# Kernel tuning notes

Measured on AMD Instinct MI355X. Metric: run time of the kernel, lower is better.

The kernel has to match this reference:

```python
import jax, jax.numpy as jnp
import numpy as np

EMBED_DIM = 128
NUM_HEADS = 4
HEAD_DIM = EMBED_DIM // NUM_HEADS


def setup_inputs() -> dict:
    key = jax.random.key(0)
    ks = jax.random.split(key, 12)
    B, N, D = 4, 4096, EMBED_DIM
    s = 1.0 / np.sqrt(D)
    inp = {
        "query": jax.random.normal(ks[0], (B, N, D), dtype=jnp.float32),
        "key": jax.random.normal(ks[1], (B, N, D), dtype=jnp.float32),
        "value": jax.random.normal(ks[2], (B, N, D), dtype=jnp.float32),
        "Wq": jax.random.uniform(ks[3], (D, D), jnp.float32, -s, s),
        "bq": jax.random.uniform(ks[4], (D,), jnp.float32, -s, s),
        "Wk": jax.random.uniform(ks[5], (D, D), jnp.float32, -s, s),
        "bk": jax.random.uniform(ks[6], (D,), jnp.float32, -s, s),
        "Wv": jax.random.uniform(ks[7], (D, D), jnp.float32, -s, s),
        "bv": jax.random.uniform(ks[8], (D,), jnp.float32, -s, s),
        "Wo": jax.random.uniform(ks[9], (D, D), jnp.float32, -s, s),
        "bo": jax.random.uniform(ks[10], (D,), jnp.float32, -s, s),
    }
    return inp


def reference(query, key, value, Wq, bq, Wk, bk, Wv, bv, Wo, bo):
    B, N, D = query.shape
    H, Dh = NUM_HEADS, HEAD_DIM
    scale = Dh ** -0.5
    # Linear projections (torch Linear: x @ W.T + b), split heads -> [B, H, N, Dh]
    Q = (query @ Wq.T + bq).reshape(B, N, H, Dh).transpose(0, 2, 1, 3)
    K = (key @ Wk.T + bk).reshape(B, N, H, Dh).transpose(0, 2, 1, 3)
    V = (value @ Wv.T + bv).reshape(B, N, H, Dh).transpose(0, 2, 1, 3)
    # Attention scores [B, H, N, N]
    scores = jnp.einsum('bhqd,bhkd->bhqk', Q, K) * scale
    attn = jax.nn.softmax(scores, axis=-1)
    ctx = jnp.einsum('bhqk,bhkd->bhqd', attn, V)  # [B, H, N, Dh]
    ctx = ctx.transpose(0, 2, 1, 3).reshape(B, N, D)
    return ctx @ Wo.T + bo
```

## Files before the change

kernel.cpp:

```cpp
#include <hip/hip_runtime.h>
#include <hip/hip_bf16.h>

#define N_SEQ 4096
#define DIM   128
#define NH    4
#define DH    32
#define BATCH 4

#define QSCALE 0.25503495870989204f

typedef __bf16 bf16x8 __attribute__((ext_vector_type(8)));
typedef __bf16 bf16x2 __attribute__((ext_vector_type(2)));
typedef __bf16 bf16x4 __attribute__((ext_vector_type(4)));
typedef float  f32x4  __attribute__((ext_vector_type(4)));

#define MFMA(a, b, c) __builtin_amdgcn_mfma_f32_16x16x32_bf16((a), (b), (c), 0, 0, 0)

static __device__ __forceinline__ bf16x8 cvt8(const float* __restrict__ p) {
    const float4* f4 = reinterpret_cast<const float4*>(p);
    float4 a = f4[0], b = f4[1];
    bf16x8 r;
    r[0] = (__bf16)a.x; r[1] = (__bf16)a.y; r[2] = (__bf16)a.z; r[3] = (__bf16)a.w;
    r[4] = (__bf16)b.x; r[5] = (__bf16)b.y; r[6] = (__bf16)b.z; r[7] = (__bf16)b.w;
    return r;
}

static __device__ __forceinline__ f32x4 exp4(f32x4 s) {
    f32x4 r;
    r[0] = __builtin_amdgcn_exp2f(s[0]);
    r[1] = __builtin_amdgcn_exp2f(s[1]);
    r[2] = __builtin_amdgcn_exp2f(s[2]);
    r[3] = __builtin_amdgcn_exp2f(s[3]);
    return r;
}

static __device__ __forceinline__ bf16x8 pack8(f32x4 a, f32x4 b) {
    bf16x8 o;
    o[0] = (__bf16)a[0]; o[1] = (__bf16)a[1];
    o[2] = (__bf16)a[2]; o[3] = (__bf16)a[3];
    o[4] = (__bf16)b[0]; o[5] = (__bf16)b[1];
    o[6] = (__bf16)b[2]; o[7] = (__bf16)b[3];
    return o;
}

__global__ __launch_bounds__(256) void cvt_w(
    const float* __restrict__ Wq, const float* __restrict__ Wk,
    const float* __restrict__ Wv, const float* __restrict__ Wo,
    __bf16* __restrict__ Wb)
{
    const int i = blockIdx.x * 256 + threadIdx.x;
    const int w = i >> 11;
    const int off = (i & 2047) * 8;
    const float* s = (w == 0) ? Wq : ((w == 1) ? Wk : ((w == 2) ? Wv : Wo));
    *(bf16x8*)(Wb + w * 16384 + off) = cvt8(s + off);
}

__global__ __launch_bounds__(256) void proj_qkv(
    const float* __restrict__ xq, const float* __restrict__ xk, const float* __restrict__ xv,
    const __bf16* __restrict__ Wb,
    const float* __restrict__ bq, const float* __restrict__ bk, const float* __restrict__ bv,
    __bf16* __restrict__ Qs, __bf16* __restrict__ Kb, __bf16* __restrict__ Vt)
{
    const int z = blockIdx.z;
    const float* x    = (z == 0) ? xq : ((z == 1) ? xk : xv);
    const __bf16* Wf  = Wb + z * 16384;
    const float* bias = (z == 0) ? bq : ((z == 1) ? bk : bv);
    const int b    = blockIdx.y;
    const int tid  = threadIdx.x;
    const int wave = tid >> 6, lane = tid & 63;
    const int quad = lane >> 4, l15 = lane & 15;
    const int n0   = blockIdx.x * 64 + wave * 16;

    bf16x8 a[4];
    const float* xrow = x + (b * N_SEQ + n0 + l15) * DIM + quad * 8;
    a[0] = cvt8(xrow);      a[1] = cvt8(xrow + 32);
    a[2] = cvt8(xrow + 64); a[3] = cvt8(xrow + 96);

    const int n = n0 + l15;
    #pragma unroll
    for (int t = 0; t < 8; t++) {
        const __bf16* wr = Wf + (t * 16 + l15) * DIM + quad * 8;
        bf16x8 w0 = *(const bf16x8*)(wr);
        bf16x8 w1 = *(const bf16x8*)(wr + 32);
        bf16x8 w2 = *(const bf16x8*)(wr + 64);
        bf16x8 w3 = *(const bf16x8*)(wr + 96);

        f32x4 acc = {0.f, 0.f, 0.f, 0.f};
        acc = MFMA(w0, a[0], acc);
        acc = MFMA(w1, a[1], acc);
        acc = MFMA(w2, a[2], acc);
        acc = MFMA(w3, a[3], acc);

        const int d0 = t * 16 + quad * 4;
        if (z == 0) {
            const int h = d0 >> 5, dh0 = d0 & 31;
            bf16x4 q4;
            #pragma unroll
            for (int r = 0; r < 4; r++)
                q4[r] = (__bf16)((acc[r] + bias[d0 + r]) * QSCALE);
            *(bf16x4*)(Qs + ((b * NH + h) * N_SEQ + n) * DH + dh0) = q4;
        } else if (z == 1) {
            const int h = d0 >> 5, dh0 = d0 & 31;
            bf16x4 k4;
            #pragma unroll
            for (int r = 0; r < 4; r++)
                k4[r] = (__bf16)(acc[r] + bias[d0 + r]);
            *(bf16x4*)(Kb + ((b * NH + h) * N_SEQ + n) * DH + dh0) = k4;
        } else {
            const int nl = n & 63;
            const int np = (n & ~63) | (nl & 35) | ((nl & 12) << 1) | ((nl & 16) >> 2);
            #pragma unroll
            for (int r = 0; r < 4; r++) {
                const int d = d0 + r, h = d >> 5, dh = d & 31;
                Vt[((b * NH + h) * DH + dh) * N_SEQ + np] = (__bf16)(acc[r] + bias[d]);
            }
        }
    }
}

__global__ __launch_bounds__(256, 2) void flash_attn(
    const __bf16* __restrict__ Qs, const __bf16* __restrict__ Kb,
    const __bf16* __restrict__ Vt, __bf16* __restrict__ ctxb)
{
    __shared__ __align__(16) char smem[77824];
    char* const Kbase = smem;
    char* const Vbase = smem + 40960;

    const int bid  = blockIdx.x;
    const int bh   = bid & 15;
    const int qc   = bid >> 4;
    const int tid  = threadIdx.x;
    const int wave = tid >> 6, lane = tid & 63;
    const int quad = lane >> 4, l15 = lane & 15;
    const int qh   = wave & 1, kh = wave >> 1;
    const int n0   = qc * 128 + qh * 64;
    const int KH   = 2048;

    const __bf16* Qp = Qs + (bh * N_SEQ + n0) * DH;
    bf16x8 qf[4];
    #pragma unroll
    for (int q = 0; q < 4; q++)
        qf[q] = *(const bf16x8*)(Qp + (q * 16 + l15) * DH + quad * 8);

    bf16x8 ones;
    #pragma unroll
    for (int i = 0; i < 8; i++) ones[i] = (__bf16)1.0f;

    const int r_ = tid >> 2, c_ = tid & 3;
    const __bf16* gK = Kb + (size_t)bh * N_SEQ * DH + r_ * DH + c_ * 8;
    const __bf16* gV = Vt + ((size_t)bh * DH + (tid >> 3)) * N_SEQ + (tid & 7) * 8;
    const int kofsK = r_ * 80 + c_ * 16;
    const int kofsV = (tid >> 3) * 144 + (tid & 7) * 16;

    {
        #pragma unroll
        for (int g = 0; g < 2; g++) {
            #pragma unroll
            for (int t = 0; t < 2; t++) {
                bf16x8 kr = *(const bf16x8*)(gK + (size_t)(g * KH + t * 64) * DH);
                bf16x8 vr = *(const bf16x8*)(gV + g * KH + t * 64);
                *(bf16x8*)(Kbase + g * 20480 + t * 5120 + kofsK) = kr;
                *(bf16x8*)(Vbase + g * 18432 + t * 4608 + kofsV) = vr;
            }
        }
    }
    __syncthreads();

    char* const Kme = Kbase + kh * 20480;
    char* const Vme = Vbase + kh * 18432;

    f32x4 c[4][2];
    f32x4 cl[4];
    const f32x4 z4 = {0.f,0.f,0.f,0.f};
    #pragma unroll
    for (int q = 0; q < 4; q++) { c[q][0] = z4; c[q][1] = z4; cl[q] = z4; }

    for (int kbb = 0; kbb < KH / 128; kbb++) {
        const int cur = kbb & 1;
        const char* Kc = Kme + cur * 10240;
        const char* Vc = Vme + cur * 9216;

        const int kn = (kbb + 1) & (KH / 128 - 1);
        bf16x8 krn[2][2], vrn[2][2];
        #pragma unroll
        for (int g = 0; g < 2; g++) {
            #pragma unroll
            for (int t = 0; t < 2; t++) {
                krn[g][t] = *(const bf16x8*)(gK + (size_t)(g * KH + kn * 128 + t * 64) * DH);
                vrn[g][t] = *(const bf16x8*)(gV + g * KH + kn * 128 + t * 64);
            }
        }

        bf16x8 kfa[2][4], vfa[2][4];
        #pragma unroll
        for (int t = 0; t < 2; t++) {
            const char* Kt  = Kc + t * 5120;
            const char* Vtl = Vc + t * 4608;
            #pragma unroll
            for (int i = 0; i < 4; i++)
                kfa[t][i] = *(const bf16x8*)(Kt + (i * 16 + l15) * 80 + quad * 16);
            vfa[t][0] = *(const bf16x8*)(Vtl + l15 * 144 + quad * 16);
            vfa[t][1] = *(const bf16x8*)(Vtl + (16 + l15) * 144 + quad * 16);
            vfa[t][2] = *(const bf16x8*)(Vtl + l15 * 144 + 64 + quad * 16);
            vfa[t][3] = *(const bf16x8*)(Vtl + (16 + l15) * 144 + 64 + quad * 16);
        }

        #pragma unroll
        for (int t = 0; t < 2; t++) {
            bf16x8 pf[4][2];
            #pragma unroll
            for (int q = 0; q < 4; q++) {
                __builtin_amdgcn_s_setprio(1);
                f32x4 sa = MFMA(kfa[t][0], qf[q], z4);
                f32x4 sb = MFMA(kfa[t][1], qf[q], z4);
                f32x4 sc = MFMA(kfa[t][2], qf[q], z4);
                f32x4 sd = MFMA(kfa[t][3], qf[q], z4);
                __builtin_amdgcn_s_setprio(0);
                f32x4 ea = exp4(sa), eb = exp4(sb), ec = exp4(sc), ed = exp4(sd);
                pf[q][0] = pack8(ea, eb);
                pf[q][1] = pack8(ec, ed);
            }

            __builtin_amdgcn_s_setprio(1);
            #pragma unroll
            for (int q = 0; q < 4; q++) {
                c[q][0] = MFMA(vfa[t][0], pf[q][0], c[q][0]);
                c[q][1] = MFMA(vfa[t][1], pf[q][0], c[q][1]);
                c[q][0] = MFMA(vfa[t][2], pf[q][1], c[q][0]);
                c[q][1] = MFMA(vfa[t][3], pf[q][1], c[q][1]);
                cl[q]   = MFMA(ones, pf[q][0], cl[q]);
                cl[q]   = MFMA(ones, pf[q][1], cl[q]);
            }
            __builtin_amdgcn_s_setprio(0);
        }

        #pragma unroll
        for (int g = 0; g < 2; g++) {
            #pragma unroll
            for (int t = 0; t < 2; t++) {
                *(bf16x8*)(Kbase + g * 20480 + (cur ^ 1) * 10240 + t * 5120 + kofsK) = krn[g][t];
                *(bf16x8*)(Vbase + g * 18432 + (cur ^ 1) * 9216 + t * 4608 + kofsV) = vrn[g][t];
            }
        }
        __syncthreads();
    }

    if (kh == 1) {
        char* dst = smem + (qh * 64 + lane) * 144;
        #pragma unroll
        for (int q = 0; q < 4; q++) {
            *(f32x4*)(dst + (q * 2 + 0) * 16) = c[q][0];
            *(f32x4*)(dst + (q * 2 + 1) * 16) = c[q][1];
        }
        f32x4 lv = {cl[0][0], cl[1][0], cl[2][0], cl[3][0]};
        *(f32x4*)(dst + 128) = lv;
    }
    __syncthreads();
    if (kh == 0) {
        const char* src = smem + (qh * 64 + lane) * 144;
        f32x4 lp = *(const f32x4*)(src + 128);
        const int b = bh >> 2, h = bh & 3;
        #pragma unroll
        for (int q = 0; q < 4; q++) {
            c[q][0] += *(const f32x4*)(src + (q * 2 + 0) * 16);
            c[q][1] += *(const f32x4*)(src + (q * 2 + 1) * 16);
            const float inv = 1.0f / (cl[q][0] + lp[q]);
            const int qg = n0 + q * 16 + l15;
            __bf16* dst = ctxb + ((size_t)(b * N_SEQ + qg)) * DIM + h * DH + quad * 4;
            #pragma unroll
            for (int dt = 0; dt < 2; dt++) {
                f32x4 cc = c[q][dt];
                bf16x2 e0 = {(__bf16)(cc[0] * inv), (__bf16)(cc[1] * inv)};
                bf16x2 e1 = {(__bf16)(cc[2] * inv), (__bf16)(cc[3] * inv)};
                *(bf16x2*)(dst + dt * 16)     = e0;
                *(bf16x2*)(dst + dt * 16 + 2) = e1;
            }
        }
    }
}

__global__ __launch_bounds__(256) void out_proj(
    const __bf16* __restrict__ ctxb, const __bf16* __restrict__ Wb,
    const float* __restrict__ bo, float* __restrict__ out)
{
    const __bf16* Wf = Wb + 3 * 16384;
    const int b    = blockIdx.y;
    const int tid  = threadIdx.x;
    const int wave = tid >> 6, lane = tid & 63;
    const int quad = lane >> 4, l15 = lane & 15;
    const int n0   = blockIdx.x * 64 + wave * 16;

    bf16x8 a[4];
    const __bf16* crow = ctxb + (b * N_SEQ + n0 + l15) * DIM + quad * 8;
    a[0] = *(const bf16x8*)(crow);
    a[1] = *(const bf16x8*)(crow + 32);
    a[2] = *(const bf16x8*)(crow + 64);
    a[3] = *(const bf16x8*)(crow + 96);

    const int n = n0 + l15;
    #pragma unroll
    for (int t = 0; t < 8; t++) {
        const __bf16* wr = Wf + (t * 16 + l15) * DIM + quad * 8;
        bf16x8 w0 = *(const bf16x8*)(wr);
        bf16x8 w1 = *(const bf16x8*)(wr + 32);
        bf16x8 w2 = *(const bf16x8*)(wr + 64);
        bf16x8 w3 = *(const bf16x8*)(wr + 96);

        f32x4 acc = {0.f, 0.f, 0.f, 0.f};
        acc = MFMA(w0, a[0], acc);
        acc = MFMA(w1, a[1], acc);
        acc = MFMA(w2, a[2], acc);
        acc = MFMA(w3, a[3], acc);

        const int d0 = t * 16 + quad * 4;
        float4 o;
        o.x = acc[0] + bo[d0];
        o.y = acc[1] + bo[d0 + 1];
        o.z = acc[2] + bo[d0 + 2];
        o.w = acc[3] + bo[d0 + 3];
        *(float4*)(out + (b * N_SEQ + n) * DIM + d0) = o;
    }
}

extern "C" void kernel_launch(void* const* d_in, const int* in_sizes, int n_in,
                              void* d_out, int out_size, void* d_ws, size_t ws_size,
                              hipStream_t stream)
{
    const float* query = (const float*)d_in[0];
    const float* key   = (const float*)d_in[1];
    const float* value = (const float*)d_in[2];
    const float* Wq = (const float*)d_in[3];
    const float* bq = (const float*)d_in[4];
    const float* Wk = (const float*)d_in[5];
    const float* bk = (const float*)d_in[6];
    const float* Wv = (const float*)d_in[7];
    const float* bv = (const float*)d_in[8];
    const float* Wo = (const float*)d_in[9];
    const float* bo = (const float*)d_in[10];
    float* out = (float*)d_out;

    char* ws = (char*)d_ws;
    const size_t e = (size_t)BATCH * N_SEQ * DIM;
    __bf16* Qs   = (__bf16*)(ws);
    __bf16* Kb   = (__bf16*)(ws + 2 * e);
    __bf16* Vt   = (__bf16*)(ws + 4 * e);
    __bf16* ctxb = (__bf16*)(ws + 6 * e);
    __bf16* Wbf  = (__bf16*)(ws + 8 * e);

    cvt_w<<<dim3(32), 256, 0, stream>>>(Wq, Wk, Wv, Wo, Wbf);
    proj_qkv<<<dim3(64, BATCH, 3), 256, 0, stream>>>(
        query, key, value, Wbf, bq, bk, bv, Qs, Kb, Vt);
    flash_attn<<<dim3(512), 256, 0, stream>>>(Qs, Kb, Vt, ctxb);
    out_proj<<<dim3(64, BATCH), 256, 0, stream>>>(ctxb, Wbf, bo, out);
}
```

Before: 154.6 us.

## Fuse weight conversion, projections, attention and output projection into one cooperative kernel

Replaces the four separate launches with a single cooperative kernel of 512 blocks that uses grid-wide syncs between the weight conversion, QKV projection, flash attention and output projection phases. The aim is to remove per-kernel launch overhead and the gaps between dependent kernels. The cost is three grid barriers, which force every block to wait for the slowest one, plus a 76KB shared-memory footprint that must still fit two blocks per CU for the cooperative launch to succeed. If the cooperative launch fails, the original four-kernel path runs instead.

```diff
diff --git a/kernel.cpp b/kernel.cpp
--- a/kernel.cpp
+++ b/kernel.cpp
@@ -1,5 +1,8 @@
 #include <hip/hip_runtime.h>
 #include <hip/hip_bf16.h>
+#include <hip/hip_cooperative_groups.h>
+
+namespace cg = cooperative_groups;
 
 #define N_SEQ 4096
 #define DIM   128
@@ -41,6 +44,284 @@
     o[4] = (__bf16)b[0]; o[5] = (__bf16)b[1];
     o[6] = (__bf16)b[2]; o[7] = (__bf16)b[3];
     return o;
+}
+
+__global__ __launch_bounds__(256, 2) void mha_fused(
+    const float* __restrict__ xq, const float* __restrict__ xk, const float* __restrict__ xv,
+    const float* __restrict__ Wq, const float* __restrict__ Wk, const float* __restrict__ Wv,
+    const float* __restrict__ Wo,
+    const float* __restrict__ bq, const float* __restrict__ bk, const float* __restrict__ bv,
+    const float* __restrict__ bo,
+    __bf16* __restrict__ Qs, __bf16* __restrict__ Kb, __bf16* __restrict__ Vt,
+    __bf16* __restrict__ ctxb, __bf16* __restrict__ Wb, float* __restrict__ out)
+{
+    __shared__ __align__(16) char smem[77824];
+    const int bid  = blockIdx.x;
+    const int tid  = threadIdx.x;
+    const int wave = tid >> 6, lane = tid & 63;
+    const int quad = lane >> 4, l15 = lane & 15;
+
+    {
+        const int gid = bid * 256 + tid;
+        if (gid < 8192) {
+            const int w = gid >> 11, off = (gid & 2047) * 8;
+            const float* s = (w == 0) ? Wq : ((w == 1) ? Wk : ((w == 2) ? Wv : Wo));
+            *(bf16x8*)(Wb + w * 16384 + off) = cvt8(s + off);
+        }
+    }
+    __threadfence();
+    cg::this_grid().sync();
+
+    for (int u = bid; u < 768; u += 512) {
+        const int z = u >> 8, rem = u & 255;
+        const int b = rem >> 6, xc = rem & 63;
+        const float* x    = (z == 0) ? xq : ((z == 1) ? xk : xv);
+        const __bf16* Wf  = Wb + z * 16384;
+        const float* bias = (z == 0) ? bq : ((z == 1) ? bk : bv);
+        const int n0 = xc * 64 + wave * 16;
+
+        bf16x8 a[4];
+        const float* xrow = x + (b * N_SEQ + n0 + l15) * DIM + quad * 8;
+        a[0] = cvt8(xrow);      a[1] = cvt8(xrow + 32);
+        a[2] = cvt8(xrow + 64); a[3] = cvt8(xrow + 96);
+
+        const int n = n0 + l15;
+        #pragma unroll
+        for (int t = 0; t < 8; t++) {
+            const __bf16* wr = Wf + (t * 16 + l15) * DIM + quad * 8;
+            bf16x8 w0 = *(const bf16x8*)(wr);
+            bf16x8 w1 = *(const bf16x8*)(wr + 32);
+            bf16x8 w2 = *(const bf16x8*)(wr + 64);
+            bf16x8 w3 = *(const bf16x8*)(wr + 96);
+
+            f32x4 acc = {0.f, 0.f, 0.f, 0.f};
+            acc = MFMA(w0, a[0], acc);
+            acc = MFMA(w1, a[1], acc);
+            acc = MFMA(w2, a[2], acc);
+            acc = MFMA(w3, a[3], acc);
+
+            const int d0 = t * 16 + quad * 4;
+            if (z == 0) {
+                const int h = d0 >> 5, dh0 = d0 & 31;
+                bf16x4 q4;
+                #pragma unroll
+                for (int r = 0; r < 4; r++)
+                    q4[r] = (__bf16)((acc[r] + bias[d0 + r]) * QSCALE);
+                *(bf16x4*)(Qs + ((b * NH + h) * N_SEQ + n) * DH + dh0) = q4;
+            } else if (z == 1) {
+                const int h = d0 >> 5, dh0 = d0 & 31;
+                bf16x4 k4;
+                #pragma unroll
+                for (int r = 0; r < 4; r++)
+                    k4[r] = (__bf16)(acc[r] + bias[d0 + r]);
+                *(bf16x4*)(Kb + ((b * NH + h) * N_SEQ + n) * DH + dh0) = k4;
+            } else {
+                const int nl = n & 63;
+                const int np = (n & ~63) | (nl & 35) | ((nl & 12) << 1) | ((nl & 16) >> 2);
+                #pragma unroll
+                for (int r = 0; r < 4; r++) {
+                    const int d = d0 + r, h = d >> 5, dh = d & 31;
+                    Vt[((b * NH + h) * DH + dh) * N_SEQ + np] = (__bf16)(acc[r] + bias[d]);
+                }
+            }
+        }
+    }
+    __threadfence();
+    cg::this_grid().sync();
+
+    {
+        char* const Kbase = smem;
+        char* const Vbase = smem + 40960;
+
+        const int bh = bid & 15;
+        const int qc = bid >> 4;
+        const int qh = wave & 1, kh = wave >> 1;
+        const int n0 = qc * 128 + qh * 64;
+        const int KH = 2048;
+
+        const __bf16* Qp = Qs + (bh * N_SEQ + n0) * DH;
+        bf16x8 qf[4];
+        #pragma unroll
+        for (int q = 0; q < 4; q++)
+            qf[q] = *(const bf16x8*)(Qp + (q * 16 + l15) * DH + quad * 8);
+
+        bf16x8 ones;
+        #pragma unroll
+        for (int i = 0; i < 8; i++) ones[i] = (__bf16)1.0f;
+
+        const int r_ = tid >> 2, c_ = tid & 3;
+        const __bf16* gK = Kb + (size_t)bh * N_SEQ * DH + r_ * DH + c_ * 8;
+        const __bf16* gV = Vt + ((size_t)bh * DH + (tid >> 3)) * N_SEQ + (tid & 7) * 8;
+        const int kofsK = r_ * 80 + c_ * 16;
+        const int kofsV = (tid >> 3) * 144 + (tid & 7) * 16;
+
+        {
+            #pragma unroll
+            for (int g = 0; g < 2; g++) {
+                #pragma unroll
+                for (int t = 0; t < 2; t++) {
+                    bf16x8 kr = *(const bf16x8*)(gK + (size_t)(g * KH + t * 64) * DH);
+                    bf16x8 vr = *(const bf16x8*)(gV + g * KH + t * 64);
+                    *(bf16x8*)(Kbase + g * 20480 + t * 5120 + kofsK) = kr;
+                    *(bf16x8*)(Vbase + g * 18432 + t * 4608 + kofsV) = vr;
+                }
+            }
+        }
+        __syncthreads();
+
+        char* const Kme = Kbase + kh * 20480;
+        char* const Vme = Vbase + kh * 18432;
+
+        f32x4 c[4][2];
+        f32x4 cl[4];
+        const f32x4 z4 = {0.f,0.f,0.f,0.f};
+        #pragma unroll
+        for (int q = 0; q < 4; q++) { c[q][0] = z4; c[q][1] = z4; cl[q] = z4; }
+
+        for (int kbb = 0; kbb < KH / 128; kbb++) {
+            const int cur = kbb & 1;
+            const char* Kc = Kme + cur * 10240;
+            const char* Vc = Vme + cur * 9216;
+
+            const int kn = (kbb + 1) & (KH / 128 - 1);
+            bf16x8 krn[2][2], vrn[2][2];
+            #pragma unroll
+            for (int g = 0; g < 2; g++) {
+                #pragma unroll
+                for (int t = 0; t < 2; t++) {
+                    krn[g][t] = *(const bf16x8*)(gK + (size_t)(g * KH + kn * 128 + t * 64) * DH);
+                    vrn[g][t] = *(const bf16x8*)(gV + g * KH + kn * 128 + t * 64);
+                }
+            }
+
+            bf16x8 kfa[2][4], vfa[2][4];
+            #pragma unroll
+            for (int t = 0; t < 2; t++) {
+                const char* Kt  = Kc + t * 5120;
+                const char* Vtl = Vc + t * 4608;
+                #pragma unroll
+                for (int i = 0; i < 4; i++)
+                    kfa[t][i] = *(const bf16x8*)(Kt + (i * 16 + l15) * 80 + quad * 16);
+                vfa[t][0] = *(const bf16x8*)(Vtl + l15 * 144 + quad * 16);
+                vfa[t][1] = *(const bf16x8*)(Vtl + (16 + l15) * 144 + quad * 16);
+                vfa[t][2] = *(const bf16x8*)(Vtl + l15 * 144 + 64 + quad * 16);
+                vfa[t][3] = *(const bf16x8*)(Vtl + (16 + l15) * 144 + 64 + quad * 16);
+            }
+
+            #pragma unroll
+            for (int t = 0; t < 2; t++) {
+                bf16x8 pf[4][2];
+                #pragma unroll
+                for (int q = 0; q < 4; q++) {
+                    __builtin_amdgcn_s_setprio(1);
+                    f32x4 sa = MFMA(kfa[t][0], qf[q], z4);
+                    f32x4 sb = MFMA(kfa[t][1], qf[q], z4);
+                    f32x4 sc = MFMA(kfa[t][2], qf[q], z4);
+                    f32x4 sd = MFMA(kfa[t][3], qf[q], z4);
+                    __builtin_amdgcn_s_setprio(0);
+                    f32x4 ea = exp4(sa), eb = exp4(sb), ec = exp4(sc), ed = exp4(sd);
+                    pf[q][0] = pack8(ea, eb);
+                    pf[q][1] = pack8(ec, ed);
+                }
+
+                __builtin_amdgcn_s_setprio(1);
+                #pragma unroll
+                for (int q = 0; q < 4; q++) {
+                    c[q][0] = MFMA(vfa[t][0], pf[q][0], c[q][0]);
+                    c[q][1] = MFMA(vfa[t][1], pf[q][0], c[q][1]);
+                    c[q][0] = MFMA(vfa[t][2], pf[q][1], c[q][0]);
+                    c[q][1] = MFMA(vfa[t][3], pf[q][1], c[q][1]);
+                    cl[q]   = MFMA(ones, pf[q][0], cl[q]);
+                    cl[q]   = MFMA(ones, pf[q][1], cl[q]);
+                }
+                __builtin_amdgcn_s_setprio(0);
+            }
+
+            #pragma unroll
+            for (int g = 0; g < 2; g++) {
+                #pragma unroll
+                for (int t = 0; t < 2; t++) {
+                    *(bf16x8*)(Kbase + g * 20480 + (cur ^ 1) * 10240 + t * 5120 + kofsK) = krn[g][t];
+                    *(bf16x8*)(Vbase + g * 18432 + (cur ^ 1) * 9216 + t * 4608 + kofsV) = vrn[g][t];
+                }
+            }
+            __syncthreads();
+        }
+
+        if (kh == 1) {
+            char* dst = smem + (qh * 64 + lane) * 144;
+            #pragma unroll
+            for (int q = 0; q < 4; q++) {
+                *(f32x4*)(dst + (q * 2 + 0) * 16) = c[q][0];
+                *(f32x4*)(dst + (q * 2 + 1) * 16) = c[q][1];
+            }
+            f32x4 lv = {cl[0][0], cl[1][0], cl[2][0], cl[3][0]};
+            *(f32x4*)(dst + 128) = lv;
+        }
+        __syncthreads();
+        if (kh == 0) {
+            const char* src = smem + (qh * 64 + lane) * 144;
+            f32x4 lp = *(const f32x4*)(src + 128);
+            const int b = bh >> 2, h = bh & 3;
+            #pragma unroll
+            for (int q = 0; q < 4; q++) {
+                c[q][0] += *(const f32x4*)(src + (q * 2 + 0) * 16);
+                c[q][1] += *(const f32x4*)(src + (q * 2 + 1) * 16);
+                const float inv = 1.0f / (cl[q][0] + lp[q]);
+                const int qg = n0 + q * 16 + l15;
+                __bf16* dst = ctxb + ((size_t)(b * N_SEQ + qg)) * DIM + h * DH + quad * 4;
+                #pragma unroll
+                for (int dt = 0; dt < 2; dt++) {
+                    f32x4 cc = c[q][dt];
+                    bf16x2 e0 = {(__bf16)(cc[0] * inv), (__bf16)(cc[1] * inv)};
+                    bf16x2 e1 = {(__bf16)(cc[2] * inv), (__bf16)(cc[3] * inv)};
+                    *(bf16x2*)(dst + dt * 16)     = e0;
+                    *(bf16x2*)(dst + dt * 16 + 2) = e1;
+                }
+            }
+        }
+    }
+    __threadfence();
+    cg::this_grid().sync();
+
+    {
+        const int nchunk = bid >> 1, thalf = bid & 1;
+        const int b = nchunk >> 6, nc = nchunk & 63;
+        const int n0 = nc * 64 + wave * 16;
+        const __bf16* Wf = Wb + 3 * 16384;
+
+        bf16x8 a[4];
+        const __bf16* crow = ctxb + (b * N_SEQ + n0 + l15) * DIM + quad * 8;
+        a[0] = *(const bf16x8*)(crow);
+        a[1] = *(const bf16x8*)(crow + 32);
+        a[2] = *(const bf16x8*)(crow + 64);
+        a[3] = *(const bf16x8*)(crow + 96);
+
+        const int n = n0 + l15;
+        #pragma unroll
+        for (int tt = 0; tt < 4; tt++) {
+            const int t = thalf * 4 + tt;
+            const __bf16* wr = Wf + (t * 16 + l15) * DIM + quad * 8;
+            bf16x8 w0 = *(const bf16x8*)(wr);
+            bf16x8 w1 = *(const bf16x8*)(wr + 32);
+            bf16x8 w2 = *(const bf16x8*)(wr + 64);
+            bf16x8 w3 = *(const bf16x8*)(wr + 96);
+
+            f32x4 acc = {0.f, 0.f, 0.f, 0.f};
+            acc = MFMA(w0, a[0], acc);
+            acc = MFMA(w1, a[1], acc);
+            acc = MFMA(w2, a[2], acc);
+            acc = MFMA(w3, a[3], acc);
+
+            const int d0 = t * 16 + quad * 4;
+            float4 o;
+            o.x = acc[0] + bo[d0];
+            o.y = acc[1] + bo[d0 + 1];
+            o.z = acc[2] + bo[d0 + 2];
+            o.w = acc[3] + bo[d0 + 3];
+            *(float4*)(out + (b * N_SEQ + n) * DIM + d0) = o;
+        }
+    }
 }
 
 __global__ __launch_bounds__(256) void cvt_w(
@@ -347,9 +628,21 @@
     __bf16* ctxb = (__bf16*)(ws + 6 * e);
     __bf16* Wbf  = (__bf16*)(ws + 8 * e);
 
-    cvt_w<<<dim3(32), 256, 0, stream>>>(Wq, Wk, Wv, Wo, Wbf);
-    proj_qkv<<<dim3(64, BATCH, 3), 256, 0, stream>>>(
-        query, key, value, Wbf, bq, bk, bv, Qs, Kb, Vt);
-    flash_attn<<<dim3(512), 256, 0, stream>>>(Qs, Kb, Vt, ctxb);
-    out_proj<<<dim3(64, BATCH), 256, 0, stream>>>(ctxb, Wbf, bo, out);
-}
+    void* args[] = {
+        (void*)&query, (void*)&key, (void*)&value,
+        (void*)&Wq, (void*)&Wk, (void*)&Wv, (void*)&Wo,
+        (void*)&bq, (void*)&bk, (void*)&bv, (void*)&bo,
+        (void*)&Qs, (void*)&Kb, (void*)&Vt, (void*)&ctxb, (void*)&Wbf,
+        (void*)&out
+    };
+    hipError_t err = hipLaunchCooperativeKernel(
+        (const void*)mha_fused, dim3(512), dim3(256), args, 0, stream);
+
+    if (err != hipSuccess) {
+        cvt_w<<<dim3(32), 256, 0, stream>>>(Wq, Wk, Wv, Wo, Wbf);
+        proj_qkv<<<dim3(64, BATCH, 3), 256, 0, stream>>>(
+            query, key, value, Wbf, bq, bk, bv, Qs, Kb, Vt);
+        flash_attn<<<dim3(512), 256, 0, stream>>>(Qs, Kb, Vt, ctxb);
+        out_proj<<<dim3(64, BATCH), 256, 0, stream>>>(ctxb, Wbf, bo, out);
+    }
+}
```

Measured after the change: 485.9 us. +214.4%, slower.
